# Performance work log

Hardware: AMD Instinct MI355X
Metric: run time of the kernel (lower is better)

## Reference

```python
import jax, jax.numpy as jnp
import numpy as np

N_NODES = 100_000
N_EDGES = 800_000
HIDDEN = 150
EDGE_FEAT = 7
N_LAYERS = 4
N_GRAPHS = 128
OUT_DIM = 6
BN_EPS = 1e-5


def setup_inputs() -> dict:
    key = jax.random.key(0)
    ks = jax.random.split(key, 16)
    x = jnp.zeros((N_NODES,), dtype=jnp.int32)  # Embedding(1, D) -> all indices 0
    edge_index = jax.random.randint(ks[0], (2, N_EDGES), 0, N_NODES, dtype=jnp.int32)
    edge_attr = jax.random.normal(ks[1], (N_EDGES, EDGE_FEAT), dtype=jnp.float32)
    batch = jnp.sort(jax.random.randint(ks[2], (N_NODES,), 0, N_GRAPHS, dtype=jnp.int32))
    s = 0.05
    node_emb = jax.random.normal(ks[3], (1, HIDDEN), dtype=jnp.float32) * s
    Wl = jax.random.normal(ks[4], (N_LAYERS, HIDDEN, HIDDEN), dtype=jnp.float32) * s
    bl = jnp.zeros((N_LAYERS, HIDDEN), dtype=jnp.float32)
    We = jax.random.normal(ks[5], (N_LAYERS, EDGE_FEAT, HIDDEN), dtype=jnp.float32) * s
    be = jnp.zeros((N_LAYERS, HIDDEN), dtype=jnp.float32)
    root = jax.random.normal(ks[6], (N_LAYERS, 1, HIDDEN), dtype=jnp.float32) * s
    gamma = jnp.ones((N_LAYERS, HIDDEN), dtype=jnp.float32)
    beta = jnp.zeros((N_LAYERS, HIDDEN), dtype=jnp.float32)
    Wp = jax.random.normal(ks[7], (HIDDEN, OUT_DIM), dtype=jnp.float32) * s
    bp = jnp.zeros((OUT_DIM,), dtype=jnp.float32)
    return {"x": x, "edge_index": edge_index, "edge_attr": edge_attr, "batch": batch,
            "node_emb": node_emb, "Wl": Wl, "bl": bl, "We": We, "be": be,
            "root": root, "gamma": gamma, "beta": beta, "Wp": Wp, "bp": bp}


def reference(x, edge_index, edge_attr, batch, node_emb, Wl, bl, We, be, root, gamma, beta, Wp, bp):
    n = x.shape[0]
    row, col = edge_index[0], edge_index[1]  # j=source, i=target (PyG default flow)
    # degree over row (as in GCNConv.forward), +1
    deg = jax.ops.segment_sum(jnp.ones((row.shape[0],), edge_attr.dtype), row, num_segments=n) + 1.0
    dis = deg ** -0.5  # deg >= 1, no inf
    norm = dis[row] * dis[col]  # [E]

    h = node_emb[x]  # [N, D]
    for l in range(N_LAYERS):
        xl = h @ Wl[l] + bl[l]                      # linear
        e = edge_attr @ We[l] + be[l]               # edge encoder
        msg = norm[:, None] * jax.nn.relu(xl[row] + e)      # per-edge message [E, D]
        agg = jax.ops.segment_sum(msg, col, num_segments=n)  # scatter-add to targets
        out = agg + jax.nn.relu(xl + root[l]) / deg[:, None]
        # BatchNorm1d (training-mode batch statistics; dropout disabled = eval)
        mu = out.mean(axis=0)
        var = out.var(axis=0)
        out = gamma[l] * (out - mu) * jax.lax.rsqrt(var + BN_EPS) + beta[l]
        if l < N_LAYERS - 1:
            out = jax.nn.relu(out)
        h = out + h  # residual=True

    # global mean pool over graphs
    counts = jax.ops.segment_sum(jnp.ones((n,), h.dtype), batch, num_segments=N_GRAPHS)
    hg = jax.ops.segment_sum(h, batch, num_segments=N_GRAPHS) / jnp.maximum(counts, 1.0)[:, None]
    return hg @ Wp + bp  # [G, OUT_DIM]
```

## Files before the change

kernel.cpp:

```cpp
#include <hip/hip_runtime.h>

#define HID 150
#define LD  160
#define NN  100000
#define NNP 100096
#define NE  800000
#define NG  128
#define NL  4
#define ODIM 6
#define BN_EPS 1e-5f
#define NSLICE 32
#define NB_SCAN 98

typedef __attribute__((ext_vector_type(8))) short short8;
typedef __attribute__((ext_vector_type(4))) float f32x4;

__device__ __forceinline__ unsigned short f2bf(float f) {
    union { float f; unsigned int u; } v; v.f = f;
    unsigned int u = v.u;
    unsigned int r = (u + 0x7FFFu + ((u >> 16) & 1u)) >> 16;
    return (unsigned short)r;
}
__device__ __forceinline__ float bf2f(unsigned short h) {
    union { unsigned int u; float f; } v; v.u = ((unsigned int)h) << 16;
    return v.f;
}

#if defined(__has_builtin)
#if __has_builtin(__builtin_amdgcn_fdot2_f32_bf16)
#define HAS_DOT2BF 1
#endif
#endif
#ifdef HAS_DOT2BF
typedef __attribute__((ext_vector_type(2))) __bf16 bf16x2;
#endif
__device__ __forceinline__ float dot2bf(unsigned int a, unsigned int b, float c) {
#ifdef HAS_DOT2BF
    union { unsigned int u; bf16x2 v; } ua, ub;
    ua.u = a; ub.u = b;
    return __builtin_amdgcn_fdot2_f32_bf16(ua.v, ub.v, c, false);
#else
    return fmaf(bf2f((unsigned short)(a & 0xffffu)), bf2f((unsigned short)(b & 0xffffu)),
           fmaf(bf2f((unsigned short)(a >> 16)), bf2f((unsigned short)(b >> 16)), c));
#endif
}

__global__ __launch_bounds__(256) void k_deg_count(const int* __restrict__ erow,
                                                   const int* __restrict__ ecol,
                                                   int* __restrict__ degi,
                                                   int* __restrict__ indeg) {
    int e = blockIdx.x * 256 + threadIdx.x;
    if (e < NE) {
        atomicAdd(&degi[erow[e]], 1);
        atomicAdd(&indeg[ecol[e]], 1);
    }
}

__global__ __launch_bounds__(256) void k_deg_fin(const int* __restrict__ degi,
                                                 float* __restrict__ degf,
                                                 float* __restrict__ dis) {
    int n = blockIdx.x * 256 + threadIdx.x;
    if (n < NN) {
        float dg = (float)degi[n] + 1.0f;
        degf[n] = dg;
        dis[n] = rsqrtf(dg);
    }
}

__global__ __launch_bounds__(1024) void k_scanA(const int* __restrict__ in,
                                                int* __restrict__ part,
                                                int* __restrict__ btot) {
    const int tid = threadIdx.x;
    const int lane = tid & 63, wave = tid >> 6;
    const int i = blockIdx.x * 1024 + tid;
    int v = (i < NN) ? in[i] : 0;
    int x = v;
#pragma unroll
    for (int o = 1; o < 64; o <<= 1) {
        int t = __shfl_up(x, o);
        if (lane >= o) x += t;
    }
    __shared__ int wsum[16];
    __shared__ int blocktot;
    if (lane == 63) wsum[wave] = x;
    __syncthreads();
    if (tid < 16) {
        int t = wsum[tid];
        int y = t;
#pragma unroll
        for (int o = 1; o < 16; o <<= 1) {
            int u = __shfl_up(y, o);
            if (tid >= o) y += u;
        }
        wsum[tid] = y - t;
        if (tid == 15) blocktot = y;
    }
    __syncthreads();
    int excl = x - v + wsum[wave];
    if (i < NN) part[i] = excl;
    if (tid == 0) btot[blockIdx.x] = blocktot;
}

__global__ __launch_bounds__(128) void k_scanB(int* __restrict__ btot) {
    const int tid = threadIdx.x;
    const int lane = tid & 63;
    int v = (tid < NB_SCAN) ? btot[tid] : 0;
    int x = v;
#pragma unroll
    for (int o = 1; o < 64; o <<= 1) {
        int t = __shfl_up(x, o);
        if (lane >= o) x += t;
    }
    __shared__ int w2;
    if (tid == 63) w2 = x;
    __syncthreads();
    int ex = x - v + ((tid >= 64) ? w2 : 0);
    if (tid < NB_SCAN) btot[tid] = ex;
}

__global__ __launch_bounds__(256) void k_scanC(int* __restrict__ coff,
                                               const int* __restrict__ btot,
                                               int* __restrict__ cursor) {
    int i = blockIdx.x * 256 + threadIdx.x;
    if (i < NN) {
        int v = coff[i] + btot[i >> 10];
        coff[i] = v;
        cursor[i] = v;
    }
    if (i == 0) coff[NN] = NE;
}

__global__ __launch_bounds__(256) void k_csr_fill(const int* __restrict__ erow,
                                                  const int* __restrict__ ecol,
                                                  const float* __restrict__ ea,
                                                  const float* __restrict__ dis,
                                                  int* __restrict__ cursor,
                                                  int2* __restrict__ csrn,
                                                  uint4* __restrict__ ceab) {
    int e = blockIdx.x * 256 + threadIdx.x;
    if (e >= NE) return;
    const int c = ecol[e], r = erow[e];
    const int p = atomicAdd(&cursor[c], 1);
    int2 m; m.x = r; m.y = __float_as_int(dis[r] * dis[c]);
    csrn[p] = m;
    const float a0 = ea[e * 7 + 0], a1 = ea[e * 7 + 1], a2 = ea[e * 7 + 2],
                a3 = ea[e * 7 + 3], a4 = ea[e * 7 + 4], a5 = ea[e * 7 + 5],
                a6 = ea[e * 7 + 6];
    uint4 A;
    A.x = (unsigned)f2bf(a0) | ((unsigned)f2bf(a1) << 16);
    A.y = (unsigned)f2bf(a2) | ((unsigned)f2bf(a3) << 16);
    A.z = (unsigned)f2bf(a4) | ((unsigned)f2bf(a5) << 16);
    A.w = (unsigned)f2bf(a6);
    ceab[p] = A;
}

__global__ __launch_bounds__(256) void k_wpack(const float* __restrict__ Wl,
                                               unsigned short* __restrict__ Wp) {
    int t = blockIdx.x * 256 + threadIdx.x;
    if (t >= 12800) return;
    const int lane = t & 63;
    const int ct = (t >> 6) % 10;
    const int ks = ((t >> 6) / 10) % 5;
    const int l = t / (64 * 10 * 5);
    const int col = ct * 16 + (lane & 15);
    const int kbase = ks * 32 + (lane >> 4) * 8;
    unsigned short v[8];
#pragma unroll
    for (int j = 0; j < 8; ++j) {
        const int k = kbase + j;
        const float f = (k < HID && col < HID) ? Wl[(size_t)l * HID * HID + k * HID + col] : 0.f;
        v[j] = f2bf(f);
    }
    *(uint4*)(Wp + (size_t)t * 8) = *(const uint4*)v;
}

__global__ __launch_bounds__(256) void k_init_h(const int* __restrict__ x,
                                                const float* __restrict__ emb,
                                                float* __restrict__ h) {
    int idx = blockIdx.x * 256 + threadIdx.x;
    if (idx >= NNP * LD) return;
    int n = idx / LD;
    int d = idx - n * LD;
    float v = 0.f;
    if (n < NN && d < HID) v = emb[x[n] * HID + d];
    h[idx] = v;
}

__global__ __launch_bounds__(256) void k_gemm(float* __restrict__ h,
                                              const unsigned short* __restrict__ obuf,
                                              const float* __restrict__ ssb,
                                              const unsigned short* __restrict__ Wp,
                                              const float* __restrict__ bias,
                                              unsigned short* __restrict__ xlb,
                                              int fuse) {
    __shared__ unsigned short Bs[5 * 10 * 64 * 8];
    {
        const uint4* src = (const uint4*)Wp;
        uint4* dst = (uint4*)Bs;
        for (int i = threadIdx.x; i < 3200; i += 256) dst[i] = src[i];
    }
    __syncthreads();

    const int wave = threadIdx.x >> 6;
    const int lane = threadIdx.x & 63;
    const int row0 = (blockIdx.x * 4 + wave) * 16;
    const int rlo = lane & 15;
    const int khi = lane >> 4;
    const int row = row0 + rlo;
    const bool rowok = row < NN;

    short8 a[5];
    if (fuse) {
#pragma unroll
        for (int ks = 0; ks < 5; ++ks) {
            const int kf = ks * 32 + khi * 8;
            const size_t base = (size_t)row * LD + kf;
            const short8 ov = *(const short8*)(obuf + base);
            const float4 h0 = *(const float4*)(h + base);
            const float4 h1 = *(const float4*)(h + base + 4);
            const float4 s0 = *(const float4*)(ssb + kf);
            const float4 s1 = *(const float4*)(ssb + kf + 4);
            const float4 t0 = *(const float4*)(ssb + LD + kf);
            const float4 t1 = *(const float4*)(ssb + LD + kf + 4);
            float hv[8];
#pragma unroll
            for (int j = 0; j < 4; ++j) {
                const bool ok = rowok && (kf + j < HID);
                const float o = bf2f((unsigned short)ov[j]);
                hv[j] = ok ? ((&h0.x)[j] + fmaxf(o * (&s0.x)[j] + (&t0.x)[j], 0.f)) : 0.f;
            }
#pragma unroll
            for (int j = 0; j < 4; ++j) {
                const bool ok = rowok && (kf + 4 + j < HID);
                const float o = bf2f((unsigned short)ov[4 + j]);
                hv[4 + j] = ok ? ((&h1.x)[j] + fmaxf(o * (&s1.x)[j] + (&t1.x)[j], 0.f)) : 0.f;
            }
            float4 w0, w1;
            w0.x = hv[0]; w0.y = hv[1]; w0.z = hv[2]; w0.w = hv[3];
            w1.x = hv[4]; w1.y = hv[5]; w1.z = hv[6]; w1.w = hv[7];
            *(float4*)(h + base) = w0;
            *(float4*)(h + base + 4) = w1;
            short8 av;
#pragma unroll
            for (int j = 0; j < 8; ++j) av[j] = (short)f2bf(hv[j]);
            a[ks] = av;
        }
    } else {
#pragma unroll
        for (int ks = 0; ks < 5; ++ks) {
            const int kf = ks * 32 + khi * 8;
            const size_t base = (size_t)row * LD + kf;
            const float4 h0 = *(const float4*)(h + base);
            const float4 h1 = *(const float4*)(h + base + 4);
            short8 av;
#pragma unroll
            for (int j = 0; j < 4; ++j) av[j] = (short)f2bf((&h0.x)[j]);
#pragma unroll
            for (int j = 0; j < 4; ++j) av[4 + j] = (short)f2bf((&h1.x)[j]);
            a[ks] = av;
        }
    }

    f32x4 acc[10];
#pragma unroll
    for (int ct = 0; ct < 10; ++ct) acc[ct] = (f32x4){0.f, 0.f, 0.f, 0.f};

    const short8* bs = (const short8*)Bs;
#pragma unroll
    for (int ks = 0; ks < 5; ++ks) {
#pragma unroll
        for (int ct = 0; ct < 10; ++ct) {
            acc[ct] = __builtin_amdgcn_mfma_f32_16x16x32_bf16(
                a[ks], bs[(ks * 10 + ct) * 64 + lane], acc[ct], 0, 0, 0);
        }
    }

#pragma unroll
    for (int ct = 0; ct < 10; ++ct) {
        const int col = ct * 16 + rlo;
        if (col < HID) {
            const float b = bias[col];
#pragma unroll
            for (int jj = 0; jj < 4; ++jj) {
                const int orow = row0 + khi * 4 + jj;
                xlb[(size_t)orow * LD + col] = f2bf(acc[ct][jj] + b);
            }
        }
    }
}

__global__ __launch_bounds__(256) void k_agg(const int* __restrict__ coff,
                                             const int2* __restrict__ csrn,
                                             const uint4* __restrict__ ceab,
                                             const float* __restrict__ We,
                                             const float* __restrict__ be,
                                             const float* __restrict__ root,
                                             const float* __restrict__ degf,
                                             const unsigned short* __restrict__ xlb,
                                             unsigned short* __restrict__ out,
                                             float* __restrict__ sums) {
    const int lane = threadIdx.x & 63;
    const int gw = (blockIdx.x * 256 + threadIdx.x) >> 6;
    const int nw = (gridDim.x * 256) >> 6;
    const int f0 = lane * 2;
    const bool tl = lane < 11;
    const int ft = tl ? (128 + lane * 2) : 128;

    unsigned wa[4], wb[4], wta[4], wtb[4];
    float bea, beb, bet0, bet1, rta, rtb, rtt0, rtt1;
#pragma unroll
    for (int p = 0; p < 3; ++p) {
        wa[p] = (unsigned)f2bf(We[(2 * p) * HID + f0]) | ((unsigned)f2bf(We[(2 * p + 1) * HID + f0]) << 16);
        wb[p] = (unsigned)f2bf(We[(2 * p) * HID + f0 + 1]) | ((unsigned)f2bf(We[(2 * p + 1) * HID + f0 + 1]) << 16);
        wta[p] = tl ? ((unsigned)f2bf(We[(2 * p) * HID + ft]) | ((unsigned)f2bf(We[(2 * p + 1) * HID + ft]) << 16)) : 0u;
        wtb[p] = tl ? ((unsigned)f2bf(We[(2 * p) * HID + ft + 1]) | ((unsigned)f2bf(We[(2 * p + 1) * HID + ft + 1]) << 16)) : 0u;
    }
    wa[3] = (unsigned)f2bf(We[6 * HID + f0]);
    wb[3] = (unsigned)f2bf(We[6 * HID + f0 + 1]);
    wta[3] = tl ? (unsigned)f2bf(We[6 * HID + ft]) : 0u;
    wtb[3] = tl ? (unsigned)f2bf(We[6 * HID + ft + 1]) : 0u;
    bea = be[f0]; beb = be[f0 + 1];
    bet0 = tl ? be[ft] : 0.f; bet1 = tl ? be[ft + 1] : 0.f;
    rta = root[f0]; rtb = root[f0 + 1];
    rtt0 = tl ? root[ft] : 0.f; rtt1 = tl ? root[ft + 1] : 0.f;

    float sa = 0.f, sb = 0.f, st0 = 0.f, st1 = 0.f;
    float qa = 0.f, qb = 0.f, qt0 = 0.f, qt1 = 0.f;

#define ENC(AA, WW, CC) dot2bf((AA).x, (WW)[0], dot2bf((AA).y, (WW)[1], dot2bf((AA).z, (WW)[2], dot2bf((AA).w, (WW)[3], (CC)))))
#define ACC_EDGE(MM, AA, XM, XT)                                                     \
    do {                                                                             \
        const float nrm = __int_as_float((MM).y);                                    \
        const float e0 = ENC(AA, wa, bea);                                           \
        const float e1 = ENC(AA, wb, beb);                                           \
        acc_a += nrm * fmaxf(bf2f((unsigned short)((XM) & 0xffffu)) + e0, 0.f);      \
        acc_b += nrm * fmaxf(bf2f((unsigned short)((XM) >> 16)) + e1, 0.f);          \
        if (tl) {                                                                    \
            const float e2 = ENC(AA, wta, bet0);                                     \
            const float e3 = ENC(AA, wtb, bet1);                                     \
            acc_t0 += nrm * fmaxf(bf2f((unsigned short)((XT) & 0xffffu)) + e2, 0.f); \
            acc_t1 += nrm * fmaxf(bf2f((unsigned short)((XT) >> 16)) + e3, 0.f);     \
        }                                                                            \
    } while (0)

    for (int i = gw; i < NN; i += nw) {
        const int j1 = coff[i + 1];
        int j = coff[i];
        float acc_a = 0.f, acc_b = 0.f, acc_t0 = 0.f, acc_t1 = 0.f;
        for (; j + 4 <= j1; j += 4) {
            const int2 m0 = csrn[j], m1 = csrn[j + 1], m2 = csrn[j + 2], m3 = csrn[j + 3];
            const uint4 A0 = ceab[j], A1 = ceab[j + 1], A2 = ceab[j + 2], A3 = ceab[j + 3];
            const unsigned short* p0 = xlb + (size_t)m0.x * LD;
            const unsigned short* p1 = xlb + (size_t)m1.x * LD;
            const unsigned short* p2 = xlb + (size_t)m2.x * LD;
            const unsigned short* p3 = xlb + (size_t)m3.x * LD;
            const unsigned x0m = *(const unsigned*)(p0 + f0);
            const unsigned x1m = *(const unsigned*)(p1 + f0);
            const unsigned x2m = *(const unsigned*)(p2 + f0);
            const unsigned x3m = *(const unsigned*)(p3 + f0);
            const unsigned x0t = tl ? *(const unsigned*)(p0 + ft) : 0u;
            const unsigned x1t = tl ? *(const unsigned*)(p1 + ft) : 0u;
            const unsigned x2t = tl ? *(const unsigned*)(p2 + ft) : 0u;
            const unsigned x3t = tl ? *(const unsigned*)(p3 + ft) : 0u;
            ACC_EDGE(m0, A0, x0m, x0t);
            ACC_EDGE(m1, A1, x1m, x1t);
            ACC_EDGE(m2, A2, x2m, x2t);
            ACC_EDGE(m3, A3, x3m, x3t);
        }
        for (; j < j1; ++j) {
            const int2 m0 = csrn[j];
            const uint4 A0 = ceab[j];
            const unsigned short* p0 = xlb + (size_t)m0.x * LD;
            const unsigned x0m = *(const unsigned*)(p0 + f0);
            const unsigned x0t = tl ? *(const unsigned*)(p0 + ft) : 0u;
            ACC_EDGE(m0, A0, x0m, x0t);
        }

        const float inv = 1.0f / degf[i];
        const unsigned short* xi = xlb + (size_t)i * LD;
        unsigned short* op = out + (size_t)i * LD;
        const unsigned xim = *(const unsigned*)(xi + f0);
        const unsigned xit = tl ? *(const unsigned*)(xi + ft) : 0u;
        {
            const float oa = acc_a + fmaxf(bf2f((unsigned short)(xim & 0xffffu)) + rta, 0.f) * inv;
            const float ob = acc_b + fmaxf(bf2f((unsigned short)(xim >> 16)) + rtb, 0.f) * inv;
            *(unsigned*)(op + f0) = (unsigned)f2bf(oa) | ((unsigned)f2bf(ob) << 16);
            sa += oa; qa += oa * oa; sb += ob; qb += ob * ob;
        }
        if (tl) {
            const float ot0 = acc_t0 + fmaxf(bf2f((unsigned short)(xit & 0xffffu)) + rtt0, 0.f) * inv;
            const float ot1 = acc_t1 + fmaxf(bf2f((unsigned short)(xit >> 16)) + rtt1, 0.f) * inv;
            *(unsigned*)(op + ft) = (unsigned)f2bf(ot0) | ((unsigned)f2bf(ot1) << 16);
            st0 += ot0; qt0 += ot0 * ot0; st1 += ot1; qt1 += ot1 * ot1;
        }
    }
#undef ACC_EDGE
#undef ENC

    __shared__ float ls[2 * LD];
    for (int i = threadIdx.x; i < 2 * LD; i += 256) ls[i] = 0.f;
    __syncthreads();
    atomicAdd(&ls[f0], sa);
    atomicAdd(&ls[f0 + 1], sb);
    atomicAdd(&ls[LD + f0], qa);
    atomicAdd(&ls[LD + f0 + 1], qb);
    if (tl) {
        atomicAdd(&ls[ft], st0);
        atomicAdd(&ls[ft + 1], st1);
        atomicAdd(&ls[LD + ft], qt0);
        atomicAdd(&ls[LD + ft + 1], qt1);
    }
    __syncthreads();
    float* sl = sums + (size_t)(blockIdx.x & (NSLICE - 1)) * 2 * LD;
    for (int i = threadIdx.x; i < 2 * LD; i += 256) atomicAdd(&sl[i], ls[i]);
}

__global__ void k_stats(const float* __restrict__ sums, const float* __restrict__ gamma,
                        const float* __restrict__ beta, float* __restrict__ ss) {
    int d = threadIdx.x;
    if (d < HID) {
        float s = 0.f, q = 0.f;
        for (int r = 0; r < NSLICE; ++r) {
            s += sums[r * 2 * LD + d];
            q += sums[r * 2 * LD + LD + d];
        }
        const float mu = s * (1.0f / NN);
        const float var = q * (1.0f / NN) - mu * mu;
        const float inv = rsqrtf(var + BN_EPS);
        const float sc = gamma[d] * inv;
        ss[d] = sc;
        ss[LD + d] = beta[d] - mu * sc;
    } else if (d < LD) {
        ss[d] = 0.f;
        ss[LD + d] = 0.f;
    }
}

__global__ __launch_bounds__(256) void k_off(const int* __restrict__ batch,
                                             int* __restrict__ off) {
    int n = blockIdx.x * 256 + threadIdx.x;
    if (n >= NN) return;
    int b = batch[n];
    if (n == 0) {
        for (int g = 0; g <= b; ++g) off[g] = 0;
    } else {
        int pb = batch[n - 1];
        for (int g = pb + 1; g <= b; ++g) off[g] = n;
    }
    if (n == NN - 1) {
        for (int g = b + 1; g <= NG; ++g) off[g] = NN;
    }
}

__global__ __launch_bounds__(512) void k_pool(const float* __restrict__ h,
                                              const unsigned short* __restrict__ obuf,
                                              const float* __restrict__ ssb,
                                              const int* __restrict__ off,
                                              const float* __restrict__ Wp,
                                              const float* __restrict__ bp,
                                              float* __restrict__ out) {
    const int g = blockIdx.x;
    const int s = off[g], e = off[g + 1];
    const float cnt = fmaxf((float)(e - s), 1.0f);
    const int lane = threadIdx.x & 63;
    const int wave = threadIdx.x >> 6;
    const bool ok2 = lane < (HID - 128);
    const int d0 = lane, d1 = lane + 64;
    const int d2 = ok2 ? (lane + 128) : 0;

    const float sc0 = ssb[d0], sc1 = ssb[d1], sc2 = ok2 ? ssb[d2] : 0.f;
    const float sh0 = ssb[LD + d0], sh1 = ssb[LD + d1], sh2 = ok2 ? ssb[LD + d2] : 0.f;

    float sum0 = 0.f, sum1 = 0.f, sum2 = 0.f;
    for (int n = s + wave; n < e; n += 8) {
        const float* hp = h + (size_t)n * LD;
        const unsigned short* op = obuf + (size_t)n * LD;
        sum0 += hp[d0] + (bf2f(op[d0]) * sc0 + sh0);
        sum1 += hp[d1] + (bf2f(op[d1]) * sc1 + sh1);
        if (ok2) sum2 += hp[d2] + (bf2f(op[d2]) * sc2 + sh2);
    }

    __shared__ float hg[LD];
    if (threadIdx.x < LD) hg[threadIdx.x] = 0.f;
    __syncthreads();
    atomicAdd(&hg[d0], sum0);
    atomicAdd(&hg[d1], sum1);
    if (ok2) atomicAdd(&hg[d2], sum2);
    __syncthreads();

    if (wave == 0) {
        float acc[ODIM] = {0.f, 0.f, 0.f, 0.f, 0.f, 0.f};
#pragma unroll
        for (int c = 0; c < 3; ++c) {
            const int d = c * 64 + lane;
            if (d < HID) {
                const float v = hg[d] / cnt;
#pragma unroll
                for (int o = 0; o < ODIM; ++o) acc[o] = fmaf(v, Wp[d * ODIM + o], acc[o]);
            }
        }
#pragma unroll
        for (int o = 0; o < ODIM; ++o) {
            float v = acc[o];
            for (int sh = 32; sh > 0; sh >>= 1) v += __shfl_down(v, sh);
            if (lane == 0) out[g * ODIM + o] = v + bp[o];
        }
    }
}

extern "C" void kernel_launch(void* const* d_in, const int* in_sizes, int n_in,
                              void* d_out, int out_size, void* d_ws, size_t ws_size,
                              hipStream_t stream) {
    const int* x = (const int*)d_in[0];
    const int* ei = (const int*)d_in[1];
    const float* ea = (const float*)d_in[2];
    const int* batch = (const int*)d_in[3];
    const float* emb = (const float*)d_in[4];
    const float* Wl = (const float*)d_in[5];
    const float* bl = (const float*)d_in[6];
    const float* We = (const float*)d_in[7];
    const float* be = (const float*)d_in[8];
    const float* root = (const float*)d_in[9];
    const float* gamma = (const float*)d_in[10];
    const float* beta = (const float*)d_in[11];
    const float* Wp = (const float*)d_in[12];
    const float* bp = (const float*)d_in[13];
    float* out = (float*)d_out;

    const int* erow = ei;
    const int* ecol = ei + NE;

    char* ws = (char*)d_ws;
    const size_t SZ4 = (size_t)NNP * LD * 4;
    const size_t SZ2 = (size_t)NNP * LD * 2;
    float* h    = (float*)(ws);
    unsigned short* xlb  = (unsigned short*)(ws + SZ4);
    unsigned short* obuf = (unsigned short*)(ws + SZ4 + SZ2);
    unsigned short* wpk  = (unsigned short*)(ws + SZ4 + 2 * SZ2);
    char* base = ws + SZ4 + 2 * SZ2 + 204800;
    int*   degi   = (int*)(base);
    int*   indeg  = (int*)(base + 409600);
    float* degf   = (float*)(base + 819200);
    float* dis    = (float*)(base + 1228800);
    int*   coff   = (int*)(base + 1638400);
    int*   cursor = (int*)(base + 2048000);
    int*   btot   = (int*)(base + 2457600);
    float* sums   = (float*)(base + 2461696);
    float* ssb    = (float*)(base + 2502656);
    int*   goff   = (int*)(base + 2506752);
    int2*  csrn   = (int2*)(base + 2510848);
    uint4* ceab   = (uint4*)(base + 8910848);

    hipMemsetAsync(degi, 0, NN * sizeof(int), stream);
    hipMemsetAsync(indeg, 0, NN * sizeof(int), stream);
    k_deg_count<<<(NE + 255) / 256, 256, 0, stream>>>(erow, ecol, degi, indeg);
    k_deg_fin<<<(NN + 255) / 256, 256, 0, stream>>>(degi, degf, dis);
    k_scanA<<<NB_SCAN, 1024, 0, stream>>>(indeg, coff, btot);
    k_scanB<<<1, 128, 0, stream>>>(btot);
    k_scanC<<<(NN + 255) / 256, 256, 0, stream>>>(coff, btot, cursor);
    k_csr_fill<<<(NE + 255) / 256, 256, 0, stream>>>(erow, ecol, ea, dis, cursor,
                                                     csrn, ceab);
    k_wpack<<<50, 256, 0, stream>>>(Wl, wpk);
    k_init_h<<<(NNP * LD + 255) / 256, 256, 0, stream>>>(x, emb, h);

    for (int l = 0; l < NL; ++l) {
        const float* b_l = bl + (size_t)l * HID;
        const float* We_l = We + (size_t)l * 7 * HID;
        const float* be_l = be + (size_t)l * HID;
        const float* root_l = root + (size_t)l * HID;
        const float* gamma_l = gamma + (size_t)l * HID;
        const float* beta_l = beta + (size_t)l * HID;
        const unsigned short* wpk_l = wpk + (size_t)l * 25600;

        k_gemm<<<NNP / 64, 256, 0, stream>>>(h, obuf, ssb, wpk_l, b_l, xlb,
                                             (l > 0) ? 1 : 0);
        hipMemsetAsync(sums, 0, NSLICE * 2 * LD * sizeof(float), stream);
        k_agg<<<2048, 256, 0, stream>>>(coff, csrn, ceab, We_l, be_l,
                                        root_l, degf, xlb, obuf, sums);
        k_stats<<<1, 256, 0, stream>>>(sums, gamma_l, beta_l, ssb);
    }

    k_off<<<(NN + 255) / 256, 256, 0, stream>>>(batch, goff);
    k_pool<<<NG, 512, 0, stream>>>(h, obuf, ssb, goff, Wp, bp, out);
}
```

Measured before the change: 871.4 us.

## Aggregate edges in wave-wide batches over contiguous node ranges per wave

Each wavefront now owns a contiguous block of 8 target nodes and walks their combined CSR edge range in batches of 8. For each batch, edge metadata is loaded cooperatively by lanes and broadcast with shuffles, and all gathers are issued before accumulation; node boundaries are detected through a new per-edge target array written during CSR fill. The aim is more memory-level parallelism and fewer tail loops on low-degree nodes. In exchange it adds shuffle traffic, a divergent emit path for segment boundaries, an extra int array, and a fixed grid sized by node count instead of a grid-stride loop.

```diff
diff --git a/kernel.cpp b/kernel.cpp
--- a/kernel.cpp
+++ b/kernel.cpp
@@ -11,6 +11,8 @@
 #define BN_EPS 1e-5f
 #define NSLICE 32
 #define NB_SCAN 98
+#define NPW 8
+#define EB  8
 
 typedef __attribute__((ext_vector_type(8))) short short8;
 typedef __attribute__((ext_vector_type(4))) float f32x4;
@@ -136,13 +138,15 @@
                                                   const float* __restrict__ dis,
                                                   int* __restrict__ cursor,
                                                   int2* __restrict__ csrn,
-                                                  uint4* __restrict__ ceab) {
+                                                  uint4* __restrict__ ceab,
+                                                  int* __restrict__ ctgt) {
     int e = blockIdx.x * 256 + threadIdx.x;
     if (e >= NE) return;
     const int c = ecol[e], r = erow[e];
     const int p = atomicAdd(&cursor[c], 1);
     int2 m; m.x = r; m.y = __float_as_int(dis[r] * dis[c]);
     csrn[p] = m;
+    ctgt[p] = c;
     const float a0 = ea[e * 7 + 0], a1 = ea[e * 7 + 1], a2 = ea[e * 7 + 2],
                 a3 = ea[e * 7 + 3], a4 = ea[e * 7 + 4], a5 = ea[e * 7 + 5],
                 a6 = ea[e * 7 + 6];
@@ -292,6 +296,7 @@
 __global__ __launch_bounds__(256) void k_agg(const int* __restrict__ coff,
                                              const int2* __restrict__ csrn,
                                              const uint4* __restrict__ ceab,
+                                             const int* __restrict__ ctgt,
                                              const float* __restrict__ We,
                                              const float* __restrict__ be,
                                              const float* __restrict__ root,
@@ -300,8 +305,7 @@
                                              unsigned short* __restrict__ out,
                                              float* __restrict__ sums) {
     const int lane = threadIdx.x & 63;
-    const int gw = (blockIdx.x * 256 + threadIdx.x) >> 6;
-    const int nw = (gridDim.x * 256) >> 6;
+    const int w = (blockIdx.x * 256 + threadIdx.x) >> 6;
     const int f0 = lane * 2;
     const bool tl = lane < 11;
     const int ft = tl ? (128 + lane * 2) : 128;
@@ -327,75 +331,100 @@
     float sa = 0.f, sb = 0.f, st0 = 0.f, st1 = 0.f;
     float qa = 0.f, qb = 0.f, qt0 = 0.f, qt1 = 0.f;
 
-#define ENC(AA, WW, CC) dot2bf((AA).x, (WW)[0], dot2bf((AA).y, (WW)[1], dot2bf((AA).z, (WW)[2], dot2bf((AA).w, (WW)[3], (CC)))))
-#define ACC_EDGE(MM, AA, XM, XT)                                                     \
-    do {                                                                             \
-        const float nrm = __int_as_float((MM).y);                                    \
-        const float e0 = ENC(AA, wa, bea);                                           \
-        const float e1 = ENC(AA, wb, beb);                                           \
-        acc_a += nrm * fmaxf(bf2f((unsigned short)((XM) & 0xffffu)) + e0, 0.f);      \
-        acc_b += nrm * fmaxf(bf2f((unsigned short)((XM) >> 16)) + e1, 0.f);          \
-        if (tl) {                                                                    \
-            const float e2 = ENC(AA, wta, bet0);                                     \
-            const float e3 = ENC(AA, wtb, bet1);                                     \
-            acc_t0 += nrm * fmaxf(bf2f((unsigned short)((XT) & 0xffffu)) + e2, 0.f); \
-            acc_t1 += nrm * fmaxf(bf2f((unsigned short)((XT) >> 16)) + e3, 0.f);     \
-        }                                                                            \
+#define EMIT(NNODE, AA, AB, AT0, AT1)                                                     \
+    do {                                                                                  \
+        const int nn_ = (NNODE);                                                          \
+        const float inv_ = 1.0f / degf[nn_];                                              \
+        const unsigned short* xi_ = xlb + (size_t)nn_ * LD;                               \
+        const unsigned xim_ = *(const unsigned*)(xi_ + f0);                               \
+        const unsigned xit_ = tl ? *(const unsigned*)(xi_ + ft) : 0u;                     \
+        unsigned short* op_ = out + (size_t)nn_ * LD;                                     \
+        const float oa_ = (AA) + fmaxf(bf2f((unsigned short)(xim_ & 0xffffu)) + rta, 0.f) * inv_; \
+        const float ob_ = (AB) + fmaxf(bf2f((unsigned short)(xim_ >> 16)) + rtb, 0.f) * inv_;     \
+        *(unsigned*)(op_ + f0) = (unsigned)f2bf(oa_) | ((unsigned)f2bf(ob_) << 16);       \
+        sa += oa_; qa += oa_ * oa_; sb += ob_; qb += ob_ * ob_;                           \
+        if (tl) {                                                                         \
+            const float ot0_ = (AT0) + fmaxf(bf2f((unsigned short)(xit_ & 0xffffu)) + rtt0, 0.f) * inv_; \
+            const float ot1_ = (AT1) + fmaxf(bf2f((unsigned short)(xit_ >> 16)) + rtt1, 0.f) * inv_;     \
+            *(unsigned*)(op_ + ft) = (unsigned)f2bf(ot0_) | ((unsigned)f2bf(ot1_) << 16); \
+            st0 += ot0_; qt0 += ot0_ * ot0_; st1 += ot1_; qt1 += ot1_ * ot1_;             \
+        }                                                                                 \
     } while (0)
 
-    for (int i = gw; i < NN; i += nw) {
-        const int j1 = coff[i + 1];
-        int j = coff[i];
+#define ACCUM(NRM, A0, A1, A2, A3, XM, XT)                                                \
+    do {                                                                                  \
+        const float e0v = dot2bf(A0, wa[0], dot2bf(A1, wa[1], dot2bf(A2, wa[2], dot2bf(A3, wa[3], bea)))); \
+        const float e1v = dot2bf(A0, wb[0], dot2bf(A1, wb[1], dot2bf(A2, wb[2], dot2bf(A3, wb[3], beb)))); \
+        acc_a += (NRM) * fmaxf(bf2f((unsigned short)((XM) & 0xffffu)) + e0v, 0.f);        \
+        acc_b += (NRM) * fmaxf(bf2f((unsigned short)((XM) >> 16)) + e1v, 0.f);            \
+        if (tl) {                                                                         \
+            const float e2v = dot2bf(A0, wta[0], dot2bf(A1, wta[1], dot2bf(A2, wta[2], dot2bf(A3, wta[3], bet0)))); \
+            const float e3v = dot2bf(A0, wtb[0], dot2bf(A1, wtb[1], dot2bf(A2, wtb[2], dot2bf(A3, wtb[3], bet1)))); \
+            acc_t0 += (NRM) * fmaxf(bf2f((unsigned short)((XT) & 0xffffu)) + e2v, 0.f);   \
+            acc_t1 += (NRM) * fmaxf(bf2f((unsigned short)((XT) >> 16)) + e3v, 0.f);       \
+        }                                                                                 \
+    } while (0)
+
+    const int i0 = w * NPW;
+    if (i0 < NN) {
+        const int i1 = min(i0 + NPW, NN);
+        const int e0 = coff[i0], e1 = coff[i1];
         float acc_a = 0.f, acc_b = 0.f, acc_t0 = 0.f, acc_t1 = 0.f;
-        for (; j + 4 <= j1; j += 4) {
-            const int2 m0 = csrn[j], m1 = csrn[j + 1], m2 = csrn[j + 2], m3 = csrn[j + 3];
-            const uint4 A0 = ceab[j], A1 = ceab[j + 1], A2 = ceab[j + 2], A3 = ceab[j + 3];
-            const unsigned short* p0 = xlb + (size_t)m0.x * LD;
-            const unsigned short* p1 = xlb + (size_t)m1.x * LD;
-            const unsigned short* p2 = xlb + (size_t)m2.x * LD;
-            const unsigned short* p3 = xlb + (size_t)m3.x * LD;
-            const unsigned x0m = *(const unsigned*)(p0 + f0);
-            const unsigned x1m = *(const unsigned*)(p1 + f0);
-            const unsigned x2m = *(const unsigned*)(p2 + f0);
-            const unsigned x3m = *(const unsigned*)(p3 + f0);
-            const unsigned x0t = tl ? *(const unsigned*)(p0 + ft) : 0u;
-            const unsigned x1t = tl ? *(const unsigned*)(p1 + ft) : 0u;
-            const unsigned x2t = tl ? *(const unsigned*)(p2 + ft) : 0u;
-            const unsigned x3t = tl ? *(const unsigned*)(p3 + ft) : 0u;
-            ACC_EDGE(m0, A0, x0m, x0t);
-            ACC_EDGE(m1, A1, x1m, x1t);
-            ACC_EDGE(m2, A2, x2m, x2t);
-            ACC_EDGE(m3, A3, x3m, x3t);
-        }
-        for (; j < j1; ++j) {
+        int cur = i0;
+        int j = e0;
+        for (; j + EB <= e1; j += EB) {
+            const int jj = j + (lane & (EB - 1));
+            const int2 mreg = csrn[jj];
+            const uint4 Areg = ceab[jj];
+            const int treg = ctgt[jj];
+            int srcs[EB];
+#pragma unroll
+            for (int k = 0; k < EB; ++k) srcs[k] = __shfl(mreg.x, k);
+            unsigned xm[EB], xt[EB];
+#pragma unroll
+            for (int k = 0; k < EB; ++k) {
+                const unsigned short* p = xlb + (size_t)srcs[k] * LD;
+                xm[k] = *(const unsigned*)(p + f0);
+                xt[k] = tl ? *(const unsigned*)(p + ft) : 0u;
+            }
+#pragma unroll
+            for (int k = 0; k < EB; ++k) {
+                const int tk = __shfl(treg, k);
+                if (tk != cur) {
+                    EMIT(cur, acc_a, acc_b, acc_t0, acc_t1);
+                    acc_a = acc_b = acc_t0 = acc_t1 = 0.f;
+                    for (int n = cur + 1; n < tk; ++n) EMIT(n, 0.f, 0.f, 0.f, 0.f);
+                    cur = tk;
+                }
+                const float nrm = __int_as_float(__shfl(mreg.y, k));
+                const unsigned a0 = (unsigned)__shfl((int)Areg.x, k);
+                const unsigned a1 = (unsigned)__shfl((int)Areg.y, k);
+                const unsigned a2 = (unsigned)__shfl((int)Areg.z, k);
+                const unsigned a3 = (unsigned)__shfl((int)Areg.w, k);
+                ACCUM(nrm, a0, a1, a2, a3, xm[k], xt[k]);
+            }
+        }
+        for (; j < e1; ++j) {
             const int2 m0 = csrn[j];
             const uint4 A0 = ceab[j];
-            const unsigned short* p0 = xlb + (size_t)m0.x * LD;
-            const unsigned x0m = *(const unsigned*)(p0 + f0);
-            const unsigned x0t = tl ? *(const unsigned*)(p0 + ft) : 0u;
-            ACC_EDGE(m0, A0, x0m, x0t);
-        }
-
-        const float inv = 1.0f / degf[i];
-        const unsigned short* xi = xlb + (size_t)i * LD;
-        unsigned short* op = out + (size_t)i * LD;
-        const unsigned xim = *(const unsigned*)(xi + f0);
-        const unsigned xit = tl ? *(const unsigned*)(xi + ft) : 0u;
-        {
-            const float oa = acc_a + fmaxf(bf2f((unsigned short)(xim & 0xffffu)) + rta, 0.f) * inv;
-            const float ob = acc_b + fmaxf(bf2f((unsigned short)(xim >> 16)) + rtb, 0.f) * inv;
-            *(unsigned*)(op + f0) = (unsigned)f2bf(oa) | ((unsigned)f2bf(ob) << 16);
-            sa += oa; qa += oa * oa; sb += ob; qb += ob * ob;
-        }
-        if (tl) {
-            const float ot0 = acc_t0 + fmaxf(bf2f((unsigned short)(xit & 0xffffu)) + rtt0, 0.f) * inv;
-            const float ot1 = acc_t1 + fmaxf(bf2f((unsigned short)(xit >> 16)) + rtt1, 0.f) * inv;
-            *(unsigned*)(op + ft) = (unsigned)f2bf(ot0) | ((unsigned)f2bf(ot1) << 16);
-            st0 += ot0; qt0 += ot0 * ot0; st1 += ot1; qt1 += ot1 * ot1;
-        }
-    }
-#undef ACC_EDGE
-#undef ENC
+            const int tk = ctgt[j];
+            const unsigned short* p = xlb + (size_t)m0.x * LD;
+            const unsigned xm0 = *(const unsigned*)(p + f0);
+            const unsigned xt0 = tl ? *(const unsigned*)(p + ft) : 0u;
+            if (tk != cur) {
+                EMIT(cur, acc_a, acc_b, acc_t0, acc_t1);
+                acc_a = acc_b = acc_t0 = acc_t1 = 0.f;
+                for (int n = cur + 1; n < tk; ++n) EMIT(n, 0.f, 0.f, 0.f, 0.f);
+                cur = tk;
+            }
+            const float nrm = __int_as_float(m0.y);
+            ACCUM(nrm, A0.x, A0.y, A0.z, A0.w, xm0, xt0);
+        }
+        EMIT(cur, acc_a, acc_b, acc_t0, acc_t1);
+        for (int n = cur + 1; n < i1; ++n) EMIT(n, 0.f, 0.f, 0.f, 0.f);
+    }
+#undef ACCUM
+#undef EMIT
 
     __shared__ float ls[2 * LD];
     for (int i = threadIdx.x; i < 2 * LD; i += 256) ls[i] = 0.f;
@@ -550,6 +579,7 @@
     int*   goff   = (int*)(base + 2506752);
     int2*  csrn   = (int2*)(base + 2510848);
     uint4* ceab   = (uint4*)(base + 8910848);
+    int*   ctgt   = (int*)(base + 21710848);
 
     hipMemsetAsync(degi, 0, NN * sizeof(int), stream);
     hipMemsetAsync(indeg, 0, NN * sizeof(int), stream);
@@ -559,9 +589,12 @@
     k_scanB<<<1, 128, 0, stream>>>(btot);
     k_scanC<<<(NN + 255) / 256, 256, 0, stream>>>(coff, btot, cursor);
     k_csr_fill<<<(NE + 255) / 256, 256, 0, stream>>>(erow, ecol, ea, dis, cursor,
-                                                     csrn, ceab);
+                                                     csrn, ceab, ctgt);
     k_wpack<<<50, 256, 0, stream>>>(Wl, wpk);
     k_init_h<<<(NNP * LD + 255) / 256, 256, 0, stream>>>(x, emb, h);
+
+    const int nwaves = (NN + NPW - 1) / NPW;
+    const int nagg = (nwaves + 3) / 4;
 
     for (int l = 0; l < NL; ++l) {
         const float* b_l = bl + (size_t)l * HID;
@@ -575,7 +608,7 @@
         k_gemm<<<NNP / 64, 256, 0, stream>>>(h, obuf, ssb, wpk_l, b_l, xlb,
                                              (l > 0) ? 1 : 0);
         hipMemsetAsync(sums, 0, NSLICE * 2 * LD * sizeof(float), stream);
-        k_agg<<<2048, 256, 0, stream>>>(coff, csrn, ceab, We_l, be_l,
+        k_agg<<<nagg, 256, 0, stream>>>(coff, csrn, ceab, ctgt, We_l, be_l,
                                         root_l, degf, xlb, obuf, sums);
         k_stats<<<1, 256, 0, stream>>>(sums, gamma_l, beta_l, ssb);
     }
```

Result: slower. 902.4 us (+3.5%).
